# Performance work log

Hardware: AMD Instinct MI355X
Metric: run time of the kernel (lower is better)

## Reference

```python
import jax, jax.numpy as jnp
import numpy as np

NEG_SLOPE = 0.2


def setup_inputs() -> dict:
    key = jax.random.key(0)
    k1, k2, k3, k4, k5, k6 = jax.random.split(key, 6)
    N, E, IN, OUT = 100000, 1600000, 256, 32
    feat = jax.random.normal(k1, (N, IN), dtype=jnp.float32)
    W = jax.random.normal(k2, (IN, OUT), dtype=jnp.float32) * (1.0 / np.sqrt(IN))
    attn_l = jax.random.normal(k3, (OUT,), dtype=jnp.float32) * 0.1
    attn_r = jax.random.normal(k4, (OUT,), dtype=jnp.float32) * 0.1
    bias = jnp.zeros((OUT,), dtype=jnp.float32)
    src = jax.random.randint(k5, (E,), 0, N, dtype=jnp.int32)
    dst = jax.random.randint(k6, (E,), 0, N, dtype=jnp.int32)
    return {"feat": feat, "W": W, "attn_l": attn_l, "attn_r": attn_r,
            "bias": bias, "src": src, "dst": dst}


def reference(feat, W, attn_l, attn_r, bias, src, dst):
    N = feat.shape[0]
    # dense projection: [N, in] @ [in, out] -> [N, out]
    h = feat @ W
    el = h @ attn_l  # [N]
    er = h @ attn_r  # [N]
    # per-edge raw score: el[u] + er[v] for edge u->v
    e = el[src] + er[dst]  # [E]
    e = jnp.where(e > 0, e, NEG_SLOPE * e)  # leaky relu
    # edge softmax grouped by destination node (numerically stable)
    m = jax.ops.segment_max(e, dst, num_segments=N)  # [N], -inf for isolated nodes
    m = jax.lax.stop_gradient(m)
    ex = jnp.exp(e - m[dst])  # [E]
    denom = jax.ops.segment_sum(ex, dst, num_segments=N)  # [N]
    alpha = ex / denom[dst]  # [E]
    # weighted aggregation (sparse SpMM): sum_{u->v} alpha_uv * h[u]
    rst = jax.ops.segment_sum(h[src] * alpha[:, None], dst, num_segments=N)  # [N, out]
    return rst + bias
```

## Files before the change

### kernel.cpp

```cpp
#include <hip/hip_runtime.h>
#include <hip/hip_bf16.h>
#include <math.h>

#define NEG_SLOPE 0.2f
#define BUCK_BITS 5
#define BUCK_NODES 32
#define CAP 800
#define SRC_MASK 0x1FFFFFF
#define NBUK_MAX 3200

#define CBITS 8
#define CNODES 256
#define CAPC 4672
#define NC_MAX 400
#define NBIN 256

typedef __bf16 bf16x8 __attribute__((ext_vector_type(8)));
typedef __bf16 bf16x4 __attribute__((ext_vector_type(4)));
typedef float  f32x4  __attribute__((ext_vector_type(4)));

__global__ void zero_cursors(unsigned int* __restrict__ fcur,
                             unsigned int* __restrict__ ccur) {
    int idx = blockIdx.x * blockDim.x + threadIdx.x;
    if (idx < NBUK_MAX) fcur[idx] = 0u;
    if (idx < NC_MAX)   ccur[idx] = 0u;
}

__global__ __launch_bounds__(256) void gemm_bin(const float* __restrict__ feat,
                                                const float* __restrict__ W,
                                                const float* __restrict__ attn_l,
                                                const float* __restrict__ attn_r,
                                                const int* __restrict__ src,
                                                const int* __restrict__ dst,
                                                __bf16* __restrict__ hb,
                                                float* __restrict__ el,
                                                float* __restrict__ er,
                                                unsigned int* __restrict__ ccur,
                                                unsigned int* __restrict__ cbin,
                                                int N, int Ntiles, int E, int NC) {
    __shared__ bf16x8 sB[1024];
    int bid = blockIdx.x;
    int tid = threadIdx.x;
    int role, gid;
    if (bid < 2 * NBIN) { role = bid & 1; gid = bid >> 1; }
    else                { role = 0;       gid = bid - NBIN; }

    if (role == 1) {
        unsigned int* hist  = (unsigned int*)sB;
        unsigned int* cbase = hist + NC_MAX;
        int batch = (E + NBIN - 1) / NBIN;
        int b0 = gid * batch;
        int b1 = min(b0 + batch, E);
        for (int i = tid; i < NC; i += 256) hist[i] = 0;
        __syncthreads();
        for (int i = b0 + tid; i < b1; i += 256)
            atomicAdd(&hist[((unsigned)dst[i]) >> CBITS], 1u);
        __syncthreads();
        for (int i = tid; i < NC; i += 256) {
            unsigned c = hist[i];
            cbase[i] = c ? atomicAdd(&ccur[i], c) : 0u;
            hist[i] = 0;
        }
        __syncthreads();
        for (int i = b0 + tid; i < b1; i += 256) {
            int d = dst[i];
            int s = src[i];
            unsigned cb = ((unsigned)d) >> CBITS;
            unsigned r = atomicAdd(&hist[cb], 1u);
            unsigned pos = cbase[cb] + r;
            if (pos < CAPC)
                cbin[(size_t)cb * CAPC + pos] =
                    ((unsigned)(d & (CNODES - 1)) << 17) | (unsigned)s;
        }
        return;
    }

#pragma unroll
    for (int t = 0; t < 4; t++) {
        int i = tid + t * 256;
        int kt = i >> 7, nt = (i >> 6) & 1, ln = i & 63;
        int qq = ln >> 4, cc = ln & 15;
        bf16x8 v;
#pragma unroll
        for (int j = 0; j < 8; j++)
            v[j] = (__bf16)W[(kt * 32 + qq * 8 + j) * 32 + nt * 16 + cc];
        sB[i] = v;
    }
    __syncthreads();

    int wid  = gid * 4 + (tid >> 6);
    int lane = tid & 63;
    if (wid >= Ntiles) return;

    int c = lane & 15, q = lane >> 4;
    int row = wid * 16 + c;
    if (row >= N) row = N - 1;
    const f32x4* A = (const f32x4*)(feat + (size_t)row * 256 + q * 8);

    f32x4 acc0 = {0.f, 0.f, 0.f, 0.f};
    f32x4 acc1 = {0.f, 0.f, 0.f, 0.f};
#pragma unroll
    for (int kt = 0; kt < 8; kt++) {
        f32x4 a0 = __builtin_nontemporal_load(A + kt * 8);
        f32x4 a1 = __builtin_nontemporal_load(A + kt * 8 + 1);
        bf16x8 ah, al;
#pragma unroll
        for (int j = 0; j < 4; j++) {
            __bf16 h0 = (__bf16)a0[j];
            __bf16 h1 = (__bf16)a1[j];
            ah[j]     = h0;
            ah[j + 4] = h1;
            al[j]     = (__bf16)(a0[j] - (float)h0);
            al[j + 4] = (__bf16)(a1[j] - (float)h1);
        }
        bf16x8 bh0 = sB[(kt * 2 + 0) * 64 + lane];
        bf16x8 bh1 = sB[(kt * 2 + 1) * 64 + lane];
        acc0 = __builtin_amdgcn_mfma_f32_16x16x32_bf16(ah, bh0, acc0, 0, 0, 0);
        acc0 = __builtin_amdgcn_mfma_f32_16x16x32_bf16(al, bh0, acc0, 0, 0, 0);
        acc1 = __builtin_amdgcn_mfma_f32_16x16x32_bf16(ah, bh1, acc1, 0, 0, 0);
        acc1 = __builtin_amdgcn_mfma_f32_16x16x32_bf16(al, bh1, acc1, 0, 0, 0);
    }

    float alc  = attn_l[c],      arc  = attn_r[c];
    float alc2 = attn_l[c + 16], arc2 = attn_r[c + 16];
#pragma unroll
    for (int r = 0; r < 4; r++) {
        int m = wid * 16 + q * 4 + r;
        if (m < N) {
            hb[(size_t)m * 32 + c]      = (__bf16)acc0[r];
            hb[(size_t)m * 32 + 16 + c] = (__bf16)acc1[r];
        }
        float pl = acc0[r] * alc + acc1[r] * alc2;
        float pr = acc0[r] * arc + acc1[r] * arc2;
#pragma unroll
        for (int off = 8; off >= 1; off >>= 1) {
            pl += __shfl_xor(pl, off);
            pr += __shfl_xor(pr, off);
        }
        if (c == 0 && m < N) { el[m] = pl; er[m] = pr; }
    }
}

__global__ __launch_bounds__(256) void refine(const unsigned int* __restrict__ ccur,
                                              const unsigned int* __restrict__ cbin,
                                              unsigned int* __restrict__ fcur,
                                              unsigned int* __restrict__ fbin,
                                              int NC) {
    __shared__ unsigned int hist[8];
    __shared__ unsigned int basec[8];
    int blk = blockIdx.x;
    int cb = blk >> 1, seg = blk & 1;
    if (cb >= NC) return;
    int tid = threadIdx.x;
    int cnt = (int)min(ccur[cb], (unsigned)CAPC);
    int lo = (cnt * seg) >> 1;
    int hi = (cnt * (seg + 1)) >> 1;

    if (tid < 8) hist[tid] = 0;
    __syncthreads();
    const unsigned int* cp = cbin + (size_t)cb * CAPC;
    unsigned int rl[10];
    int k = 0;
    for (int i = lo + tid; i < hi; i += 256) {
        unsigned r = cp[i];
        rl[k++] = r;
        atomicAdd(&hist[(r >> (17 + BUCK_BITS)) & 7], 1u);
    }
    __syncthreads();
    if (tid < 8) {
        unsigned v = hist[tid];
        basec[tid] = v ? atomicAdd(&fcur[cb * 8 + tid], v) : 0u;
        hist[tid] = 0;
    }
    __syncthreads();
    k = 0;
    for (int i = lo + tid; i < hi; i += 256) {
        unsigned r = rl[k++];
        int fb = (r >> (17 + BUCK_BITS)) & 7;
        unsigned rank = atomicAdd(&hist[fb], 1u);
        unsigned pos = basec[fb] + rank;
        if (pos < CAP)
            fbin[(size_t)(cb * 8 + fb) * CAP + pos] =
                (((r >> 17) & (BUCK_NODES - 1)) << 25) | (r & 0x1FFFFu);
    }
}

__global__ __launch_bounds__(256) void aggregate(const unsigned int* __restrict__ cursor,
                                                 const unsigned int* __restrict__ binned,
                                                 const float* __restrict__ el,
                                                 const float* __restrict__ er,
                                                 const __bf16* __restrict__ hb,
                                                 const float* __restrict__ bias,
                                                 float* __restrict__ out, int N) {
    __shared__ uint2        rw_s[CAP];
    __shared__ unsigned int hist[BUCK_NODES];
    __shared__ int          off_s[BUCK_NODES + 1];
    __shared__ float        den[BUCK_NODES];
    __shared__ float        er_l[BUCK_NODES];

    int buck = blockIdx.x;
    int base = buck << BUCK_BITS;
    int nn = min(BUCK_NODES, N - base);
    int tid = threadIdx.x;

    int cnt = (int)min(cursor[buck], (unsigned)CAP);
    const unsigned int* eb = binned + (size_t)buck * CAP;

    if (tid < BUCK_NODES) {
        hist[tid] = 0;
        den[tid] = 0.f;
        er_l[tid] = (tid < nn) ? er[base + tid] : 0.f;
    }
    __syncthreads();

    unsigned int rl[4];
    int k = 0;
    for (int i = tid; i < cnt; i += 256) {
        unsigned r = eb[i];
        rl[k++] = r;
        atomicAdd(&hist[r >> 25], 1u);
    }
    __syncthreads();

    if (tid < BUCK_NODES) {
        int v = (int)hist[tid];
        int orig = v;
#pragma unroll
        for (int off = 1; off < BUCK_NODES; off <<= 1) {
            int x = __shfl_up(v, off, 64);
            if (tid >= off) v += x;
        }
        off_s[tid] = v - orig;
        if (tid == BUCK_NODES - 1) off_s[BUCK_NODES] = v;
        hist[tid] = (unsigned)(v - orig);
    }
    __syncthreads();

    k = 0;
    for (int i = tid; i < cnt; i += 256) {
        unsigned r = rl[k++];
        int s = r & SRC_MASK;
        int d = r >> 25;
        float e = el[s] + er_l[d];
        e = (e > 0.f) ? e : NEG_SLOPE * e;
        float w = __expf(e);
        unsigned pos = atomicAdd(&hist[d], 1u);
        rw_s[pos] = make_uint2((unsigned)s, __float_as_uint(w));
        atomicAdd(&den[d], w);
    }
    __syncthreads();

    int lane = tid & 63, wv = tid >> 6;
    int oct = lane >> 3, t = lane & 7;
    f32x4 b4 = *(const f32x4*)&bias[t * 4];
    for (int n = wv; n < nn; n += 4) {
        float sm = den[n];
        int s0 = off_s[n], s1 = off_s[n + 1];
        f32x4 acc = {0.f, 0.f, 0.f, 0.f};
#pragma unroll 2
        for (int j = s0 + oct; j < s1; j += 8) {
            uint2 rw = rw_s[j];
            float w = __uint_as_float(rw.y);
            bf16x4 hv = *(const bf16x4*)&hb[(size_t)rw.x * 32 + t * 4];
            acc[0] += w * (float)hv[0];
            acc[1] += w * (float)hv[1];
            acc[2] += w * (float)hv[2];
            acc[3] += w * (float)hv[3];
        }
#pragma unroll
        for (int off = 8; off <= 32; off <<= 1) {
            acc[0] += __shfl_xor(acc[0], off);
            acc[1] += __shfl_xor(acc[1], off);
            acc[2] += __shfl_xor(acc[2], off);
            acc[3] += __shfl_xor(acc[3], off);
        }
        if (lane < 8) {
            f32x4 o;
            if (sm > 0.f) {
                float inv = 1.f / sm;
                o[0] = acc[0] * inv + b4[0];
                o[1] = acc[1] * inv + b4[1];
                o[2] = acc[2] * inv + b4[2];
                o[3] = acc[3] * inv + b4[3];
            } else {
                o = b4;
            }
            *(f32x4*)&out[(size_t)(base + n) * 32 + t * 4] = o;
        }
    }
}

static inline size_t align256(size_t x) { return (x + 255) & ~(size_t)255; }

extern "C" void kernel_launch(void* const* d_in, const int* in_sizes, int n_in,
                              void* d_out, int out_size, void* d_ws, size_t ws_size,
                              hipStream_t stream) {
    const float* feat   = (const float*)d_in[0];
    const float* W      = (const float*)d_in[1];
    const float* attn_l = (const float*)d_in[2];
    const float* attn_r = (const float*)d_in[3];
    const float* bias   = (const float*)d_in[4];
    const int* src = (const int*)d_in[5];
    const int* dst = (const int*)d_in[6];
    float* out = (float*)d_out;

    const int IN = 256;
    int N = in_sizes[0] / IN;
    int E = in_sizes[5];
    (void)n_in; (void)out_size; (void)ws_size;

    int Ntiles = (N + 15) / 16;
    int NBUK = (N + BUCK_NODES - 1) >> BUCK_BITS;
    int NC   = (N + CNODES - 1) >> CBITS;
    int NG   = (Ntiles + 3) / 4;

    char* p = (char*)d_ws;
    __bf16* hb     = (__bf16*)p; p += align256((size_t)N * 32 * 2);
    float* el      = (float*)p; p += align256((size_t)N * 4);
    float* er      = (float*)p; p += align256((size_t)N * 4);
    unsigned int* fcur = (unsigned int*)p; p += align256((size_t)NBUK_MAX * 4);
    unsigned int* ccur = (unsigned int*)p; p += align256((size_t)NC_MAX * 4);
    unsigned int* fbin = (unsigned int*)p; p += align256((size_t)NBUK * CAP * 4);
    unsigned int* cbin = (unsigned int*)p; p += align256((size_t)NC * CAPC * 4);

    zero_cursors<<<(NBUK_MAX + 255) / 256, 256, 0, stream>>>(fcur, ccur);
    gemm_bin<<<NG + NBIN, 256, 0, stream>>>(feat, W, attn_l, attn_r, src, dst,
                                            hb, el, er, ccur, cbin,
                                            N, Ntiles, E, NC);
    refine<<<NC * 2, 256, 0, stream>>>(ccur, cbin, fcur, fbin, NC);
    aggregate<<<NBUK, 256, 0, stream>>>(fcur, fbin, el, er, hb, bias, out, N);
}
```

Before: 248.0 us.

## Drop refine pass; aggregate filters coarse bins directly and precompute bf16 W

Removes the refine kernel that split coarse 256-node bins into 32-node fine bins. Each aggregate block now scans the whole coarse bin (about 4096 edges) and keeps only the edges for its own 32-node bucket, which is an 8x read redundancy served mostly from cache. W conversion to bf16 and its layout permutation move into a small prep kernel, so each gemm block just copies the prepared tile into shared memory. This saves one kernel launch and a global write/read pass but adds redundant scanning in aggregate.

```diff
diff --git a/kernel.cpp b/kernel.cpp
--- a/kernel.cpp
+++ b/kernel.cpp
@@ -6,8 +6,6 @@
 #define BUCK_BITS 5
 #define BUCK_NODES 32
 #define CAP 800
-#define SRC_MASK 0x1FFFFFF
-#define NBUK_MAX 3200
 
 #define CBITS 8
 #define CNODES 256
@@ -19,15 +17,20 @@
 typedef __bf16 bf16x4 __attribute__((ext_vector_type(4)));
 typedef float  f32x4  __attribute__((ext_vector_type(4)));
 
-__global__ void zero_cursors(unsigned int* __restrict__ fcur,
-                             unsigned int* __restrict__ ccur) {
+__global__ void prep(const float* __restrict__ W, __bf16* __restrict__ Whi,
+                     unsigned int* __restrict__ ccur, int NC) {
     int idx = blockIdx.x * blockDim.x + threadIdx.x;
-    if (idx < NBUK_MAX) fcur[idx] = 0u;
-    if (idx < NC_MAX)   ccur[idx] = 0u;
+    if (idx < NC) ccur[idx] = 0u;
+    if (idx >= 8192) return;
+    int j = idx & 7, lane = (idx >> 3) & 63, nt = (idx >> 9) & 1, kt = idx >> 10;
+    int q = lane >> 4, c = lane & 15;
+    int k = kt * 32 + q * 8 + j;
+    int n = nt * 16 + c;
+    Whi[idx] = (__bf16)W[k * 32 + n];
 }
 
 __global__ __launch_bounds__(256) void gemm_bin(const float* __restrict__ feat,
-                                                const float* __restrict__ W,
+                                                const __bf16* __restrict__ Whi,
                                                 const float* __restrict__ attn_l,
                                                 const float* __restrict__ attn_r,
                                                 const int* __restrict__ src,
@@ -75,17 +78,7 @@
         return;
     }
 
-#pragma unroll
-    for (int t = 0; t < 4; t++) {
-        int i = tid + t * 256;
-        int kt = i >> 7, nt = (i >> 6) & 1, ln = i & 63;
-        int qq = ln >> 4, cc = ln & 15;
-        bf16x8 v;
-#pragma unroll
-        for (int j = 0; j < 8; j++)
-            v[j] = (__bf16)W[(kt * 32 + qq * 8 + j) * 32 + nt * 16 + cc];
-        sB[i] = v;
-    }
+    for (int i = tid; i < 1024; i += 256) sB[i] = ((const bf16x8*)Whi)[i];
     __syncthreads();
 
     int wid  = gid * 4 + (tid >> 6);
@@ -141,52 +134,8 @@
     }
 }
 
-__global__ __launch_bounds__(256) void refine(const unsigned int* __restrict__ ccur,
-                                              const unsigned int* __restrict__ cbin,
-                                              unsigned int* __restrict__ fcur,
-                                              unsigned int* __restrict__ fbin,
-                                              int NC) {
-    __shared__ unsigned int hist[8];
-    __shared__ unsigned int basec[8];
-    int blk = blockIdx.x;
-    int cb = blk >> 1, seg = blk & 1;
-    if (cb >= NC) return;
-    int tid = threadIdx.x;
-    int cnt = (int)min(ccur[cb], (unsigned)CAPC);
-    int lo = (cnt * seg) >> 1;
-    int hi = (cnt * (seg + 1)) >> 1;
-
-    if (tid < 8) hist[tid] = 0;
-    __syncthreads();
-    const unsigned int* cp = cbin + (size_t)cb * CAPC;
-    unsigned int rl[10];
-    int k = 0;
-    for (int i = lo + tid; i < hi; i += 256) {
-        unsigned r = cp[i];
-        rl[k++] = r;
-        atomicAdd(&hist[(r >> (17 + BUCK_BITS)) & 7], 1u);
-    }
-    __syncthreads();
-    if (tid < 8) {
-        unsigned v = hist[tid];
-        basec[tid] = v ? atomicAdd(&fcur[cb * 8 + tid], v) : 0u;
-        hist[tid] = 0;
-    }
-    __syncthreads();
-    k = 0;
-    for (int i = lo + tid; i < hi; i += 256) {
-        unsigned r = rl[k++];
-        int fb = (r >> (17 + BUCK_BITS)) & 7;
-        unsigned rank = atomicAdd(&hist[fb], 1u);
-        unsigned pos = basec[fb] + rank;
-        if (pos < CAP)
-            fbin[(size_t)(cb * 8 + fb) * CAP + pos] =
-                (((r >> 17) & (BUCK_NODES - 1)) << 25) | (r & 0x1FFFFu);
-    }
-}
-
-__global__ __launch_bounds__(256) void aggregate(const unsigned int* __restrict__ cursor,
-                                                 const unsigned int* __restrict__ binned,
+__global__ __launch_bounds__(256) void aggregate(const unsigned int* __restrict__ ccur,
+                                                 const unsigned int* __restrict__ cbin,
                                                  const float* __restrict__ el,
                                                  const float* __restrict__ er,
                                                  const __bf16* __restrict__ hb,
@@ -199,12 +148,14 @@
     __shared__ float        er_l[BUCK_NODES];
 
     int buck = blockIdx.x;
+    int cb = buck >> 3;
+    unsigned fb = (unsigned)(buck & 7);
     int base = buck << BUCK_BITS;
     int nn = min(BUCK_NODES, N - base);
     int tid = threadIdx.x;
 
-    int cnt = (int)min(cursor[buck], (unsigned)CAP);
-    const unsigned int* eb = binned + (size_t)buck * CAP;
+    int cnt_c = (int)min(ccur[cb], (unsigned)CAPC);
+    const unsigned int* cp = cbin + (size_t)cb * CAPC;
 
     if (tid < BUCK_NODES) {
         hist[tid] = 0;
@@ -213,12 +164,10 @@
     }
     __syncthreads();
 
-    unsigned int rl[4];
-    int k = 0;
-    for (int i = tid; i < cnt; i += 256) {
-        unsigned r = eb[i];
-        rl[k++] = r;
-        atomicAdd(&hist[r >> 25], 1u);
+    for (int i = tid; i < cnt_c; i += 256) {
+        unsigned r = cp[i];
+        if (((r >> 22) & 7u) == fb)
+            atomicAdd(&hist[(r >> 17) & (BUCK_NODES - 1)], 1u);
     }
     __syncthreads();
 
@@ -236,17 +185,19 @@
     }
     __syncthreads();
 
-    k = 0;
-    for (int i = tid; i < cnt; i += 256) {
-        unsigned r = rl[k++];
-        int s = r & SRC_MASK;
-        int d = r >> 25;
+    for (int i = tid; i < cnt_c; i += 256) {
+        unsigned r = cp[i];
+        if (((r >> 22) & 7u) != fb) continue;
+        int s = (int)(r & 0x1FFFFu);
+        int d = (int)((r >> 17) & (BUCK_NODES - 1));
         float e = el[s] + er_l[d];
         e = (e > 0.f) ? e : NEG_SLOPE * e;
         float w = __expf(e);
         unsigned pos = atomicAdd(&hist[d], 1u);
-        rw_s[pos] = make_uint2((unsigned)s, __float_as_uint(w));
-        atomicAdd(&den[d], w);
+        if (pos < CAP) {
+            rw_s[pos] = make_uint2((unsigned)s, __float_as_uint(w));
+            atomicAdd(&den[d], w);
+        }
     }
     __syncthreads();
 
@@ -255,7 +206,7 @@
     f32x4 b4 = *(const f32x4*)&bias[t * 4];
     for (int n = wv; n < nn; n += 4) {
         float sm = den[n];
-        int s0 = off_s[n], s1 = off_s[n + 1];
+        int s0 = min(off_s[n], CAP), s1 = min(off_s[n + 1], CAP);
         f32x4 acc = {0.f, 0.f, 0.f, 0.f};
 #pragma unroll 2
         for (int j = s0 + oct; j < s1; j += 8) {
@@ -318,15 +269,13 @@
     __bf16* hb     = (__bf16*)p; p += align256((size_t)N * 32 * 2);
     float* el      = (float*)p; p += align256((size_t)N * 4);
     float* er      = (float*)p; p += align256((size_t)N * 4);
-    unsigned int* fcur = (unsigned int*)p; p += align256((size_t)NBUK_MAX * 4);
     unsigned int* ccur = (unsigned int*)p; p += align256((size_t)NC_MAX * 4);
-    unsigned int* fbin = (unsigned int*)p; p += align256((size_t)NBUK * CAP * 4);
     unsigned int* cbin = (unsigned int*)p; p += align256((size_t)NC * CAPC * 4);
-
-    zero_cursors<<<(NBUK_MAX + 255) / 256, 256, 0, stream>>>(fcur, ccur);
-    gemm_bin<<<NG + NBIN, 256, 0, stream>>>(feat, W, attn_l, attn_r, src, dst,
+    __bf16* Whi    = (__bf16*)p; p += align256((size_t)8192 * 2);
+
+    prep<<<33, 256, 0, stream>>>(W, Whi, ccur, NC);
+    gemm_bin<<<NG + NBIN, 256, 0, stream>>>(feat, Whi, attn_l, attn_r, src, dst,
                                             hb, el, er, ccur, cbin,
                                             N, Ntiles, E, NC);
-    refine<<<NC * 2, 256, 0, stream>>>(ccur, cbin, fcur, fbin, NC);
-    aggregate<<<NBUK, 256, 0, stream>>>(fcur, fbin, el, er, hb, bias, out, N);
-}
+    aggregate<<<NBUK, 256, 0, stream>>>(ccur, cbin, el, er, hb, bias, out, N);
+}
```

Result: slower. 263.3 us (+6.2%).
